# Kernel optimization log

Measured on AMD Instinct MI355X. Metric: run time of the kernel, lower is better.

## Reference

```python
import jax, jax.numpy as jnp
import numpy as np

D_MODEL = 1024
N_HEADS = 16
D_K = D_MODEL // N_HEADS
B, S = 2, 2048


def setup_inputs() -> dict:
    key = jax.random.key(0)
    ks = jax.random.split(key, 9)
    scale = 1.0 / np.sqrt(D_MODEL)
    x = jax.random.normal(ks[0], (B, S, D_MODEL), dtype=jnp.float32)
    # causal mask, broadcastable to [B, H, S, S]; mask==0 -> masked
    mask = jnp.tril(jnp.ones((S, S), dtype=bool))[None, None]
    wq = jax.random.normal(ks[1], (D_MODEL, D_MODEL), dtype=jnp.float32) * scale
    bq = jnp.zeros((D_MODEL,), dtype=jnp.float32)
    wk = jax.random.normal(ks[2], (D_MODEL, D_K), dtype=jnp.float32) * scale
    bk = jnp.zeros((D_K,), dtype=jnp.float32)
    wv = jax.random.normal(ks[3], (D_MODEL, D_K), dtype=jnp.float32) * scale
    bv = jnp.zeros((D_K,), dtype=jnp.float32)
    wo = jax.random.normal(ks[4], (D_MODEL, D_MODEL), dtype=jnp.float32) * scale
    bo = jnp.zeros((D_MODEL,), dtype=jnp.float32)
    return {"x": x, "mask": mask, "wq": wq, "bq": bq, "wk": wk, "bk": bk,
            "wv": wv, "bv": bv, "wo": wo, "bo": bo}


def reference(x, mask, wq, bq, wk, bk, wv, bv, wo, bo):
    b, s, d = x.shape
    h, dk = N_HEADS, D_K
    q = (x @ wq + bq).reshape(b, s, h, dk)            # [b,s,h,dk]
    k = x @ wk + bk                                    # [b,s,dk] shared across heads (MQA)
    v = x @ wv + bv                                    # [b,s,dk]
    scores = jnp.einsum('bshd,btd->bhst', q, k) / jnp.sqrt(jnp.float32(dk))
    scores = jnp.where(mask, scores, jnp.float32(-1e9))
    attn = jax.nn.softmax(scores, axis=-1)             # [b,h,s,t]
    out = jnp.einsum('bhst,btd->bshd', attn, v).reshape(b, s, d)
    return out @ wo + bo
```

## Files before the change

kernel.cpp:

```cpp
#include <hip/hip_runtime.h>
#include <hip/hip_bf16.h>
#include <stdint.h>


typedef __attribute__((ext_vector_type(8))) short short8;
typedef __attribute__((ext_vector_type(4))) short short4_t;
typedef __attribute__((ext_vector_type(4))) float f32x4;

#define MFMA16(a, b, c) __builtin_amdgcn_mfma_f32_16x16x32_bf16((a), (b), (c), 0, 0, 0)

#define SCALE_Q 0.1803368801111244f

__device__ inline void gload_lds16(const void* g, void* l) {
  __builtin_amdgcn_global_load_lds(
      (const __attribute__((address_space(1))) void*)g,
      (__attribute__((address_space(3))) void*)l, 16, 0, 0);
}

__device__ inline float fast_exp2(float x) {
  float r;
  asm("v_exp_f32 %0, %1" : "=v"(r) : "v"(x));
  return r;
}

__device__ inline short f2bf(float f) {
  union { float f; uint32_t u; } v;
  v.f = f;
  uint32_t u = v.u;
  return (short)((u + 0x7fffu + ((u >> 16) & 1u)) >> 16);
}

__device__ inline uint32_t pk_bf16(float lo, float hi) {
  uint32_t r;
  asm("v_cvt_pk_bf16_f32 %0, %1, %2" : "=v"(r) : "v"(lo), "v"(hi));
  return r;
}

__device__ inline int imin(int a, int b) { return a < b ? a : b; }

__global__ __launch_bounds__(256) void k_prep(
    const float* __restrict__ x, const float* __restrict__ wq,
    const float* __restrict__ wk, const float* __restrict__ wv,
    const float* __restrict__ bq, const float* __restrict__ bk,
    const float* __restrict__ bv, const float* __restrict__ wo,
    short* __restrict__ xb, short* __restrict__ wqkvt,
    float* __restrict__ biasq, short* __restrict__ wot) {
  const int blk = blockIdx.x;
  const int t = threadIdx.x;
  if (blk >= 545) {
    const int base = (blk - 545) * 8192;
#pragma unroll
    for (int it = 0; it < 4; ++it) {
      const int i = base + it * 2048 + t * 8;
      const float* xp = x + i;
      short8 o;
#pragma unroll
      for (int j = 0; j < 8; ++j) o[j] = f2bf(xp[j]);
      *(short8*)(xb + i) = o;
    }
    return;
  }
  if (blk == 544) {
    for (int idx = t; idx < 1152; idx += 256)
      biasq[idx] = idx < 1024 ? bq[idx] * SCALE_Q
                              : (idx < 1088 ? bk[idx - 1024] : bv[idx - 1088]);
    return;
  }
  __shared__ float lds[64][65];
  const int j = blk;
  const float* src;
  short* dst;
  int ncol, k0, n0, row0;
  float sc = 1.f;
  if (j < 256)      { src = wq; dst = wqkvt; ncol = 1024; k0 = (j >> 4) * 64;
                      n0 = (j & 15) * 64; row0 = n0; sc = SCALE_Q; }
  else if (j < 272) { src = wk; dst = wqkvt; ncol = 64; k0 = (j - 256) * 64;
                      n0 = 0; row0 = 1024; }
  else if (j < 288) { src = wv; dst = wqkvt; ncol = 64; k0 = (j - 272) * 64;
                      n0 = 0; row0 = 1088; }
  else              { int jj = j - 288; src = wo; dst = wot; ncol = 1024;
                      k0 = (jj >> 4) * 64; n0 = (jj & 15) * 64; row0 = n0; }
#pragma unroll
  for (int i = 0; i < 4; ++i) {
    int f = i * 256 + t;
    int k = f >> 4, c = f & 15;
    const float* sp = src + (size_t)(k0 + k) * ncol + n0 + c * 4;
#pragma unroll
    for (int q = 0; q < 4; ++q) lds[k][c * 4 + q] = sp[q];
  }
  __syncthreads();
#pragma unroll
  for (int i = 0; i < 2; ++i) {
    int f = i * 256 + t;
    int n = f >> 3, kc = f & 7;
    short8 o;
#pragma unroll
    for (int q = 0; q < 8; ++q) o[q] = f2bf(lds[kc * 8 + q][n] * sc);
    *(short8*)(dst + (size_t)(row0 + n) * 1024 + k0 + kc * 8) = o;
  }
}

__global__ __launch_bounds__(256) void k_vt(const short* __restrict__ qkv,
                                            short* __restrict__ vt) {
  __shared__ short lds[64][72];
  const int blk = blockIdx.x;
  const int b = blk >> 5, T = blk & 31;
  const int t = threadIdx.x;
#pragma unroll
  for (int i = 0; i < 2; ++i) {
    int f = i * 256 + t;
    int row = f >> 3, c = f & 7;
    short8 v = *(const short8*)(qkv +
        (size_t)(b * 2048 + T * 64 + row) * 1152 + 1088 + c * 8);
    *(short8*)(&lds[row][c * 8]) = v;
  }
  __syncthreads();
#pragma unroll
  for (int i = 0; i < 2; ++i) {
    int f = i * 256 + t;
    int d = f & 63, g = f >> 6;
    short8 o;
#pragma unroll
    for (int j = 0; j < 8; ++j) {
      int c = g * 8 + j;
      int pi = 16 * ((c >> 1) & 3) + 4 * ((c >> 3) & 3) + 2 * (c >> 5) + (c & 1);
      o[j] = lds[pi][d];
    }
    *(short8*)(vt + (size_t)(b * 64 + d) * 2048 + T * 64 + g * 8) = o;
  }
}

__global__ __launch_bounds__(256, 3) void k_gemm(const short* __restrict__ A,
                                                 const short* __restrict__ Bt,
                                                 const float* __restrict__ bias,
                                                 void* __restrict__ C, int ldc,
                                                 int out_bf16) {
  __shared__ short As[2][4096];
  __shared__ short Bs[2][8192];
  const int t = threadIdx.x;
  const int w = t >> 6, l = t & 63;
  const int l15 = l & 15, lhi = l >> 4;
  const int m0 = blockIdx.x * 64, n0 = blockIdx.y * 128;

  f32x4 acc[4][2];
#pragma unroll
  for (int i = 0; i < 4; ++i)
#pragma unroll
    for (int j = 0; j < 2; ++j)
#pragma unroll
      for (int r = 0; r < 4; ++r) acc[i][j][r] = 0.f;

  const int fA0 = w * 64 + l;
  const int rA0 = fA0 >> 3, gA0 = (fA0 & 7) ^ (rA0 & 7);
  const int fA1 = fA0 + 256;
  const int rA1 = fA1 >> 3, gA1 = (fA1 & 7) ^ (rA1 & 7);

  const int aoff = l15 * 128 + ((lhi ^ (l15 & 7)) << 4);
  const int coff = l15 * 128 + (((4 + lhi) ^ (l15 & 7)) << 4);

#define GEMM_STAGE(buf, k0)                                                    \
  {                                                                            \
    gload_lds16(A + (size_t)(m0 + rA0) * 1024 + (k0) + gA0 * 8,               \
                &As[buf][w * 512]);                                            \
    gload_lds16(A + (size_t)(m0 + rA1) * 1024 + (k0) + gA1 * 8,               \
                &As[buf][2048 + w * 512]);                                     \
    _Pragma("unroll")                                                          \
    for (int q = 0; q < 4; ++q) {                                              \
      int f = q * 256 + fA0;                                                   \
      int r = f >> 3, gc = (f & 7) ^ (r & 7);                                  \
      gload_lds16(Bt + (size_t)(n0 + r) * 1024 + (k0) + gc * 8,               \
                  &Bs[buf][q * 2048 + w * 512]);                               \
    }                                                                          \
  }

  GEMM_STAGE(0, 0);

  for (int ks = 0; ks < 16; ++ks) {
    const int nb = (ks + 1) & 1;
    GEMM_STAGE(nb, imin(ks + 1, 15) * 64);
    asm volatile("s_waitcnt vmcnt(6)" ::: "memory");

    const char* as = (const char*)&As[ks & 1][0];
    const char* bs = (const char*)&Bs[ks & 1][0];
    short8 afA[4], afB[4], bfA[2], bfB[2];
#pragma unroll
    for (int i = 0; i < 4; ++i) {
      afA[i] = *(const short8*)(as + i * 2048 + aoff);
      afB[i] = *(const short8*)(as + i * 2048 + coff);
    }
#pragma unroll
    for (int j = 0; j < 2; ++j) {
      bfA[j] = *(const short8*)(bs + (w * 32 + j * 16) * 128 + aoff);
      bfB[j] = *(const short8*)(bs + (w * 32 + j * 16) * 128 + coff);
    }
#pragma unroll
    for (int i = 0; i < 4; ++i)
#pragma unroll
      for (int j = 0; j < 2; ++j) {
        acc[i][j] = MFMA16(afA[i], bfA[j], acc[i][j]);
        acc[i][j] = MFMA16(afB[i], bfB[j], acc[i][j]);
      }
    __builtin_amdgcn_s_barrier();
  }
  asm volatile("s_waitcnt vmcnt(0)" ::: "memory");

#pragma unroll
  for (int j = 0; j < 2; ++j) {
    int col = n0 + w * 32 + j * 16 + l15;
    float bia = bias[col];
#pragma unroll
    for (int i = 0; i < 4; ++i) {
      int row0 = m0 + i * 16 + lhi * 4;
      if (out_bf16) {
#pragma unroll
        for (int r = 0; r < 4; ++r)
          ((short*)C)[(size_t)(row0 + r) * ldc + col] =
              (short)(pk_bf16(acc[i][j][r] + bia, 0.f) & 0xffff);
      } else {
#pragma unroll
        for (int r = 0; r < 4; ++r)
          ((float*)C)[(size_t)(row0 + r) * ldc + col] = acc[i][j][r] + bia;
      }
    }
  }
#undef GEMM_STAGE
}

__global__ __launch_bounds__(512, 4) void k_attn(const short* __restrict__ qkv,
                                                 const short* __restrict__ vt,
                                                 short* __restrict__ attnb) {
  __shared__ char smem[65536];
  const int t = threadIdx.x;
  const int w = t >> 6, l = t & 63;
  const int l15 = l & 15, lhi = l >> 4;
  const int qw = w & 3, g2 = w >> 2;
  const int bx = blockIdx.x;
  const int o = bx >> 5, gg = o & 7;
  const int p = (o < 8) ? gg : 15 - gg;
  const int bh = bx & 31, b = bh >> 4, h = bh & 15;
  const int ntiles = 2 * p + 2, nph = p + 1;
  const short* kb = qkv + (size_t)(b * 2048) * 1152 + 1024;
  const short* vb = vt + (size_t)b * 64 * 2048;

  const int srow = w * 8 + (l >> 3);
  const int gcol = (l & 7) ^ (l >> 3);
  const short* kS = kb + (size_t)srow * 1152 + gcol * 8;
  const short* vS = vb + (size_t)srow * 2048 + gcol * 8;

  const int aoff = l15 * 128 + ((lhi ^ (l15 & 7)) << 4);
  const int coff = l15 * 128 + (((4 + lhi) ^ (l15 & 7)) << 4);

  short8 ones;
#pragma unroll
  for (int j = 0; j < 8; ++j) ones[j] = (short)0x3F80;

  const int qbase = p * 128 + qw * 32;
  const int myq0 = qbase + l15;
  const int myq1 = qbase + 16 + l15;
  const int ttdiag = qbase >> 6;

  const short* qp0 = qkv + (size_t)(b * 2048 + myq0) * 1152 + h * 64 + 8 * lhi;
  const short* qp1 = qkv + (size_t)(b * 2048 + myq1) * 1152 + h * 64 + 8 * lhi;
  short8 qa0 = *(const short8*)(qp0);
  short8 qc0 = *(const short8*)(qp0 + 32);
  short8 qa1 = *(const short8*)(qp1);
  short8 qc1 = *(const short8*)(qp1 + 32);

  f32x4 oo[2][4], o5a, o5b;
#pragma unroll
  for (int qg = 0; qg < 2; ++qg)
#pragma unroll
    for (int fd = 0; fd < 4; ++fd)
#pragma unroll
      for (int r = 0; r < 4; ++r) oo[qg][fd][r] = 0.f;
#pragma unroll
  for (int r = 0; r < 4; ++r) { o5a[r] = 0.f; o5b[r] = 0.f; }

  gload_lds16(kS, smem + w * 1024);
  gload_lds16(kS + 73728, smem + 16384 + w * 1024);
  gload_lds16(vS, smem + 32768 + w * 1024);
  gload_lds16(vS + 64, smem + 32768 + 16384 + w * 1024);
  __syncthreads();

#pragma unroll 1
  for (int i = 0; i < nph; ++i) {
    if (i + 1 < nph) {
      const int nb = (i + 1) & 1;
      const size_t ko2 = (size_t)(2 * i + 2) * 73728;
      const int vo2 = (2 * i + 2) * 64;
      gload_lds16(kS + ko2, smem + nb * 8192 + w * 1024);
      gload_lds16(kS + ko2 + 73728, smem + 16384 + nb * 8192 + w * 1024);
      gload_lds16(vS + vo2, smem + 32768 + nb * 8192 + w * 1024);
      gload_lds16(vS + vo2 + 64, smem + 32768 + 16384 + nb * 8192 + w * 1024);
      __builtin_amdgcn_sched_barrier(0);
    }

    const int tt = 2 * i + g2;
    const int cb = i & 1;

    const char* kr = smem + g2 * 16384 + cb * 8192;
    f32x4 s0[4], s1[4];
    __builtin_amdgcn_s_setprio(1);
#pragma unroll
    for (int f = 0; f < 4; ++f) {
      short8 ka = *(const short8*)(kr + f * 2048 + aoff);
      short8 kc = *(const short8*)(kr + f * 2048 + coff);
      f32x4 z0 = {0.f, 0.f, 0.f, 0.f};
      z0 = MFMA16(ka, qa0, z0);
      z0 = MFMA16(kc, qc0, z0);
      s0[f] = z0;
      f32x4 z1 = {0.f, 0.f, 0.f, 0.f};
      z1 = MFMA16(ka, qa1, z1);
      z1 = MFMA16(kc, qc1, z1);
      s1[f] = z1;
    }
    __builtin_amdgcn_s_setprio(0);

    if (tt >= ttdiag) {
      const int t0 = tt * 64;
#pragma unroll
      for (int f = 0; f < 4; ++f) {
        int kvb = t0 + f * 16 + lhi * 4;
#pragma unroll
        for (int r = 0; r < 4; ++r) {
          s0[f][r] = (kvb + r <= myq0) ? s0[f][r] : -1e30f;
          s1[f][r] = (kvb + r <= myq1) ? s1[f][r] : -1e30f;
        }
      }
    }

#pragma unroll
    for (int f = 0; f < 4; ++f)
#pragma unroll
      for (int r = 0; r < 4; ++r) {
        s0[f][r] = fast_exp2(s0[f][r]);
        s1[f][r] = fast_exp2(s1[f][r]);
      }

    union { short8 v; uint32_t d[4]; } pA0, pB0, pA1, pB1;
#pragma unroll
    for (int f = 0; f < 4; ++f) {
      pA0.d[f] = pk_bf16(s0[f][0], s0[f][1]);
      pB0.d[f] = pk_bf16(s0[f][2], s0[f][3]);
      pA1.d[f] = pk_bf16(s1[f][0], s1[f][1]);
      pB1.d[f] = pk_bf16(s1[f][2], s1[f][3]);
    }

    const char* vr = smem + 32768 + g2 * 16384 + cb * 8192;
    __builtin_amdgcn_s_setprio(1);
#pragma unroll
    for (int fd = 0; fd < 4; ++fd) {
      short8 va = *(const short8*)(vr + fd * 2048 + aoff);
      short8 vc = *(const short8*)(vr + fd * 2048 + coff);
      oo[0][fd] = MFMA16(va, pA0.v, oo[0][fd]);
      oo[0][fd] = MFMA16(vc, pB0.v, oo[0][fd]);
      oo[1][fd] = MFMA16(va, pA1.v, oo[1][fd]);
      oo[1][fd] = MFMA16(vc, pB1.v, oo[1][fd]);
    }
    o5a = MFMA16(ones, pA0.v, o5a);
    o5a = MFMA16(ones, pB0.v, o5a);
    o5b = MFMA16(ones, pA1.v, o5b);
    o5b = MFMA16(ones, pB1.v, o5b);
    __builtin_amdgcn_s_setprio(0);

    __syncthreads();
  }

  float* scr = (float*)smem;
  float* sp = scr + ((qw << 6) + l) * 34;
  if (g2 == 1) {
#pragma unroll
    for (int qg = 0; qg < 2; ++qg)
#pragma unroll
      for (int fd = 0; fd < 4; ++fd)
#pragma unroll
        for (int r = 0; r < 4; ++r) sp[qg * 16 + fd * 4 + r] = oo[qg][fd][r];
    sp[32] = o5a[0];
    sp[33] = o5b[0];
  }
  __syncthreads();
  if (g2 == 0) {
#pragma unroll
    for (int qg = 0; qg < 2; ++qg) {
      float lsum = (qg ? o5b[0] : o5a[0]) + sp[32 + qg];
      float inv = 1.f / lsum;
      int myq = qbase + qg * 16 + l15;
      short* op = attnb + (size_t)(b * 2048 + myq) * 1024 + h * 64;
#pragma unroll
      for (int fd = 0; fd < 4; ++fd) {
        union { short4_t s4; uint32_t d[2]; } ov;
        float v0 = (oo[qg][fd][0] + sp[qg * 16 + fd * 4 + 0]) * inv;
        float v1 = (oo[qg][fd][1] + sp[qg * 16 + fd * 4 + 1]) * inv;
        float v2 = (oo[qg][fd][2] + sp[qg * 16 + fd * 4 + 2]) * inv;
        float v3 = (oo[qg][fd][3] + sp[qg * 16 + fd * 4 + 3]) * inv;
        ov.d[0] = pk_bf16(v0, v1);
        ov.d[1] = pk_bf16(v2, v3);
        *(short4_t*)(op + fd * 16 + lhi * 4) = ov.s4;
      }
    }
  }
}

extern "C" void kernel_launch(void* const* d_in, const int* in_sizes, int n_in,
                              void* d_out, int out_size, void* d_ws, size_t ws_size,
                              hipStream_t stream) {
  const float* x  = (const float*)d_in[0];
  const float* wq = (const float*)d_in[2];
  const float* bq = (const float*)d_in[3];
  const float* wk = (const float*)d_in[4];
  const float* bk = (const float*)d_in[5];
  const float* wv = (const float*)d_in[6];
  const float* bv = (const float*)d_in[7];
  const float* wo = (const float*)d_in[8];
  const float* bo = (const float*)d_in[9];

  char* ws = (char*)d_ws;
  short* xb    = (short*)(ws + 0);
  short* qkv   = (short*)(ws + 8388608);
  short* wqkvt = (short*)(ws + 17825792);
  short* wot   = (short*)(ws + 20185088);
  short* vt    = (short*)(ws + 22282240);
  short* attnb = (short*)(ws + 22806528);
  float* biasq = (float*)(ws + 31195136);

  k_prep<<<1057, 256, 0, stream>>>(x, wq, wk, wv, bq, bk, bv, wo,
                                   xb, wqkvt, biasq, wot);
  k_gemm<<<dim3(64, 9), 256, 0, stream>>>(xb, wqkvt, biasq, qkv, 1152, 1);
  k_vt<<<64, 256, 0, stream>>>(qkv, vt);
  k_attn<<<512, 512, 0, stream>>>(qkv, vt, attnb);
  k_gemm<<<dim3(64, 8), 256, 0, stream>>>(attnb, wot, bo, d_out, 1024, 0);
}
```

Before: 71.74 us.

## Halve attention block to 4 waves, each computing 64 query rows

The attention kernel drops from 8 waves to 4 waves per block, and each wave now handles 64 query rows (four 16-row groups) instead of 32. K/V fragments loaded from LDS are reused across all four groups, which cuts LDS reads per MFMA. Each wave issues twice the global-to-LDS staging loads. The cost is much higher register pressure from 16 output accumulators plus Q fragments, and fewer waves to hide latency, with launch bounds changed to (256,2).

```diff
diff --git a/kernel.cpp b/kernel.cpp
--- a/kernel.cpp
+++ b/kernel.cpp
@@ -226,26 +226,28 @@
 #undef GEMM_STAGE
 }
 
-__global__ __launch_bounds__(512, 4) void k_attn(const short* __restrict__ qkv,
+__global__ __launch_bounds__(256, 2) void k_attn(const short* __restrict__ qkv,
                                                  const short* __restrict__ vt,
                                                  short* __restrict__ attnb) {
   __shared__ char smem[65536];
   const int t = threadIdx.x;
   const int w = t >> 6, l = t & 63;
   const int l15 = l & 15, lhi = l >> 4;
-  const int qw = w & 3, g2 = w >> 2;
+  const int qw = w & 1, g2 = w >> 1;
   const int bx = blockIdx.x;
   const int o = bx >> 5, gg = o & 7;
   const int p = (o < 8) ? gg : 15 - gg;
   const int bh = bx & 31, b = bh >> 4, h = bh & 15;
-  const int ntiles = 2 * p + 2, nph = p + 1;
+  const int nph = p + 1;
   const short* kb = qkv + (size_t)(b * 2048) * 1152 + 1024;
   const short* vb = vt + (size_t)b * 64 * 2048;
 
-  const int srow = w * 8 + (l >> 3);
+  const int srow = w * 16 + (l >> 3);
   const int gcol = (l & 7) ^ (l >> 3);
   const short* kS = kb + (size_t)srow * 1152 + gcol * 8;
   const short* vS = vb + (size_t)srow * 2048 + gcol * 8;
+  const short* kS2 = kS + (size_t)8 * 1152;
+  const short* vS2 = vS + (size_t)8 * 2048;
 
   const int aoff = l15 * 128 + ((lhi ^ (l15 & 7)) << 4);
   const int coff = l15 * 128 + (((4 + lhi) ^ (l15 & 7)) << 4);
@@ -254,44 +256,51 @@
 #pragma unroll
   for (int j = 0; j < 8; ++j) ones[j] = (short)0x3F80;
 
-  const int qbase = p * 128 + qw * 32;
-  const int myq0 = qbase + l15;
-  const int myq1 = qbase + 16 + l15;
+  const int qbase = p * 128 + qw * 64;
   const int ttdiag = qbase >> 6;
 
-  const short* qp0 = qkv + (size_t)(b * 2048 + myq0) * 1152 + h * 64 + 8 * lhi;
-  const short* qp1 = qkv + (size_t)(b * 2048 + myq1) * 1152 + h * 64 + 8 * lhi;
-  short8 qa0 = *(const short8*)(qp0);
-  short8 qc0 = *(const short8*)(qp0 + 32);
-  short8 qa1 = *(const short8*)(qp1);
-  short8 qc1 = *(const short8*)(qp1 + 32);
-
-  f32x4 oo[2][4], o5a, o5b;
-#pragma unroll
-  for (int qg = 0; qg < 2; ++qg)
+  short8 qa[4], qc[4];
+#pragma unroll
+  for (int g = 0; g < 4; ++g) {
+    const short* qp = qkv +
+        (size_t)(b * 2048 + qbase + g * 16 + l15) * 1152 + h * 64 + 8 * lhi;
+    qa[g] = *(const short8*)(qp);
+    qc[g] = *(const short8*)(qp + 32);
+  }
+
+  f32x4 oo[4][4], o5[4];
+#pragma unroll
+  for (int g = 0; g < 4; ++g) {
 #pragma unroll
     for (int fd = 0; fd < 4; ++fd)
 #pragma unroll
-      for (int r = 0; r < 4; ++r) oo[qg][fd][r] = 0.f;
-#pragma unroll
-  for (int r = 0; r < 4; ++r) { o5a[r] = 0.f; o5b[r] = 0.f; }
-
-  gload_lds16(kS, smem + w * 1024);
-  gload_lds16(kS + 73728, smem + 16384 + w * 1024);
-  gload_lds16(vS, smem + 32768 + w * 1024);
-  gload_lds16(vS + 64, smem + 32768 + 16384 + w * 1024);
+      for (int r = 0; r < 4; ++r) oo[g][fd][r] = 0.f;
+#pragma unroll
+    for (int r = 0; r < 4; ++r) o5[g][r] = 0.f;
+  }
+
+#define ASTAGE(db, tl)                                                         \
+  {                                                                            \
+    const size_t ko = (size_t)(tl) * 73728;                                    \
+    const int vo = (tl) * 64;                                                  \
+    gload_lds16(kS + ko, smem + (db) * 8192 + w * 2048);                       \
+    gload_lds16(kS2 + ko, smem + (db) * 8192 + w * 2048 + 1024);               \
+    gload_lds16(kS + ko + 73728, smem + 16384 + (db) * 8192 + w * 2048);       \
+    gload_lds16(kS2 + ko + 73728,                                              \
+                smem + 16384 + (db) * 8192 + w * 2048 + 1024);                 \
+    gload_lds16(vS + vo, smem + 32768 + (db) * 8192 + w * 2048);               \
+    gload_lds16(vS2 + vo, smem + 32768 + (db) * 8192 + w * 2048 + 1024);       \
+    gload_lds16(vS + vo + 64, smem + 49152 + (db) * 8192 + w * 2048);          \
+    gload_lds16(vS2 + vo + 64, smem + 49152 + (db) * 8192 + w * 2048 + 1024);  \
+  }
+
+  ASTAGE(0, 0);
   __syncthreads();
 
 #pragma unroll 1
   for (int i = 0; i < nph; ++i) {
     if (i + 1 < nph) {
-      const int nb = (i + 1) & 1;
-      const size_t ko2 = (size_t)(2 * i + 2) * 73728;
-      const int vo2 = (2 * i + 2) * 64;
-      gload_lds16(kS + ko2, smem + nb * 8192 + w * 1024);
-      gload_lds16(kS + ko2 + 73728, smem + 16384 + nb * 8192 + w * 1024);
-      gload_lds16(vS + vo2, smem + 32768 + nb * 8192 + w * 1024);
-      gload_lds16(vS + vo2 + 64, smem + 32768 + 16384 + nb * 8192 + w * 1024);
+      ASTAGE((i + 1) & 1, 2 * i + 2);
       __builtin_amdgcn_sched_barrier(0);
     }
 
@@ -299,51 +308,52 @@
     const int cb = i & 1;
 
     const char* kr = smem + g2 * 16384 + cb * 8192;
-    f32x4 s0[4], s1[4];
-    __builtin_amdgcn_s_setprio(1);
+    short8 ka[4], kc[4];
 #pragma unroll
     for (int f = 0; f < 4; ++f) {
-      short8 ka = *(const short8*)(kr + f * 2048 + aoff);
-      short8 kc = *(const short8*)(kr + f * 2048 + coff);
-      f32x4 z0 = {0.f, 0.f, 0.f, 0.f};
-      z0 = MFMA16(ka, qa0, z0);
-      z0 = MFMA16(kc, qc0, z0);
-      s0[f] = z0;
-      f32x4 z1 = {0.f, 0.f, 0.f, 0.f};
-      z1 = MFMA16(ka, qa1, z1);
-      z1 = MFMA16(kc, qc1, z1);
-      s1[f] = z1;
-    }
-    __builtin_amdgcn_s_setprio(0);
-
-    if (tt >= ttdiag) {
-      const int t0 = tt * 64;
+      ka[f] = *(const short8*)(kr + f * 2048 + aoff);
+      kc[f] = *(const short8*)(kr + f * 2048 + coff);
+    }
+
+    union { short8 v; uint32_t d[4]; } pA[4], pB[4];
+    const int t0 = tt * 64;
+
+#pragma unroll
+    for (int g = 0; g < 4; ++g) {
+      f32x4 s[4];
+      __builtin_amdgcn_s_setprio(1);
 #pragma unroll
       for (int f = 0; f < 4; ++f) {
-        int kvb = t0 + f * 16 + lhi * 4;
-#pragma unroll
-        for (int r = 0; r < 4; ++r) {
-          s0[f][r] = (kvb + r <= myq0) ? s0[f][r] : -1e30f;
-          s1[f][r] = (kvb + r <= myq1) ? s1[f][r] : -1e30f;
+        f32x4 z = {0.f, 0.f, 0.f, 0.f};
+        z = MFMA16(ka[f], qa[g], z);
+        z = MFMA16(kc[f], qc[g], z);
+        s[f] = z;
+      }
+      __builtin_amdgcn_s_setprio(0);
+
+      if (tt >= ttdiag) {
+        const int myq = qbase + g * 16 + l15;
+#pragma unroll
+        for (int f = 0; f < 4; ++f) {
+          int kvb = t0 + f * 16 + lhi * 4;
+#pragma unroll
+          for (int r = 0; r < 4; ++r)
+            s[f][r] = (kvb + r <= myq) ? s[f][r] : -1e30f;
         }
       }
-    }
-
-#pragma unroll
-    for (int f = 0; f < 4; ++f)
-#pragma unroll
-      for (int r = 0; r < 4; ++r) {
-        s0[f][r] = fast_exp2(s0[f][r]);
-        s1[f][r] = fast_exp2(s1[f][r]);
-      }
-
-    union { short8 v; uint32_t d[4]; } pA0, pB0, pA1, pB1;
-#pragma unroll
-    for (int f = 0; f < 4; ++f) {
-      pA0.d[f] = pk_bf16(s0[f][0], s0[f][1]);
-      pB0.d[f] = pk_bf16(s0[f][2], s0[f][3]);
-      pA1.d[f] = pk_bf16(s1[f][0], s1[f][1]);
-      pB1.d[f] = pk_bf16(s1[f][2], s1[f][3]);
+
+#pragma unroll
+      for (int f = 0; f < 4; ++f) {
+        s[f][0] = fast_exp2(s[f][0]);
+        s[f][1] = fast_exp2(s[f][1]);
+        s[f][2] = fast_exp2(s[f][2]);
+        s[f][3] = fast_exp2(s[f][3]);
+      }
+#pragma unroll
+      for (int f = 0; f < 4; ++f) {
+        pA[g].d[f] = pk_bf16(s[f][0], s[f][1]);
+        pB[g].d[f] = pk_bf16(s[f][2], s[f][3]);
+      }
     }
 
     const char* vr = smem + 32768 + g2 * 16384 + cb * 8192;
@@ -352,47 +362,50 @@
     for (int fd = 0; fd < 4; ++fd) {
       short8 va = *(const short8*)(vr + fd * 2048 + aoff);
       short8 vc = *(const short8*)(vr + fd * 2048 + coff);
-      oo[0][fd] = MFMA16(va, pA0.v, oo[0][fd]);
-      oo[0][fd] = MFMA16(vc, pB0.v, oo[0][fd]);
-      oo[1][fd] = MFMA16(va, pA1.v, oo[1][fd]);
-      oo[1][fd] = MFMA16(vc, pB1.v, oo[1][fd]);
-    }
-    o5a = MFMA16(ones, pA0.v, o5a);
-    o5a = MFMA16(ones, pB0.v, o5a);
-    o5b = MFMA16(ones, pA1.v, o5b);
-    o5b = MFMA16(ones, pB1.v, o5b);
+#pragma unroll
+      for (int g = 0; g < 4; ++g) {
+        oo[g][fd] = MFMA16(va, pA[g].v, oo[g][fd]);
+        oo[g][fd] = MFMA16(vc, pB[g].v, oo[g][fd]);
+      }
+    }
+#pragma unroll
+    for (int g = 0; g < 4; ++g) {
+      o5[g] = MFMA16(ones, pA[g].v, o5[g]);
+      o5[g] = MFMA16(ones, pB[g].v, o5[g]);
+    }
     __builtin_amdgcn_s_setprio(0);
 
     __syncthreads();
   }
+#undef ASTAGE
 
   float* scr = (float*)smem;
-  float* sp = scr + ((qw << 6) + l) * 34;
+  float* sp = scr + ((qw << 6) + l) * 68;
   if (g2 == 1) {
 #pragma unroll
-    for (int qg = 0; qg < 2; ++qg)
+    for (int g = 0; g < 4; ++g) {
 #pragma unroll
       for (int fd = 0; fd < 4; ++fd)
 #pragma unroll
-        for (int r = 0; r < 4; ++r) sp[qg * 16 + fd * 4 + r] = oo[qg][fd][r];
-    sp[32] = o5a[0];
-    sp[33] = o5b[0];
+        for (int r = 0; r < 4; ++r) sp[g * 16 + fd * 4 + r] = oo[g][fd][r];
+      sp[64 + g] = o5[g][0];
+    }
   }
   __syncthreads();
   if (g2 == 0) {
 #pragma unroll
-    for (int qg = 0; qg < 2; ++qg) {
-      float lsum = (qg ? o5b[0] : o5a[0]) + sp[32 + qg];
+    for (int g = 0; g < 4; ++g) {
+      float lsum = o5[g][0] + sp[64 + g];
       float inv = 1.f / lsum;
-      int myq = qbase + qg * 16 + l15;
+      int myq = qbase + g * 16 + l15;
       short* op = attnb + (size_t)(b * 2048 + myq) * 1024 + h * 64;
 #pragma unroll
       for (int fd = 0; fd < 4; ++fd) {
         union { short4_t s4; uint32_t d[2]; } ov;
-        float v0 = (oo[qg][fd][0] + sp[qg * 16 + fd * 4 + 0]) * inv;
-        float v1 = (oo[qg][fd][1] + sp[qg * 16 + fd * 4 + 1]) * inv;
-        float v2 = (oo[qg][fd][2] + sp[qg * 16 + fd * 4 + 2]) * inv;
-        float v3 = (oo[qg][fd][3] + sp[qg * 16 + fd * 4 + 3]) * inv;
+        float v0 = (oo[g][fd][0] + sp[g * 16 + fd * 4 + 0]) * inv;
+        float v1 = (oo[g][fd][1] + sp[g * 16 + fd * 4 + 1]) * inv;
+        float v2 = (oo[g][fd][2] + sp[g * 16 + fd * 4 + 2]) * inv;
+        float v3 = (oo[g][fd][3] + sp[g * 16 + fd * 4 + 3]) * inv;
         ov.d[0] = pk_bf16(v0, v1);
         ov.d[1] = pk_bf16(v2, v3);
         *(short4_t*)(op + fd * 16 + lhi * 4) = ov.s4;
@@ -427,6 +440,6 @@
                                    xb, wqkvt, biasq, wot);
   k_gemm<<<dim3(64, 9), 256, 0, stream>>>(xb, wqkvt, biasq, qkv, 1152, 1);
   k_vt<<<64, 256, 0, stream>>>(qkv, vt);
-  k_attn<<<512, 512, 0, stream>>>(qkv, vt, attnb);
+  k_attn<<<512, 256, 0, stream>>>(qkv, vt, attnb);
   k_gemm<<<dim3(64, 8), 256, 0, stream>>>(attnb, wot, bo, d_out, 1024, 0);
 }
```

Measured after the change: 72.79 us. No clear change (+1.5%).

## Split attention into smaller 64-query blocks with 32-key tiles and 4 waves

Applied to the files above, without the earlier changes.

The attention kernel now launches 1024 blocks of 256 threads, each handling 64 queries instead of 128. Each iteration processes two 32-key tiles instead of two 64-key tiles, and the V transpose permutation changes to match the new P fragment layout. The aim is finer-grained parallelism, better causal load balancing and lower per-block LDS so more blocks are resident. The cost is more per-block overhead, more synchronisation relative to MFMA work, and more iterations with half the MFMA work each.

```diff
diff --git a/kernel.cpp b/kernel.cpp
--- a/kernel.cpp
+++ b/kernel.cpp
@@ -123,7 +123,7 @@
 #pragma unroll
     for (int j = 0; j < 8; ++j) {
       int c = g * 8 + j;
-      int pi = 16 * ((c >> 1) & 3) + 4 * ((c >> 3) & 3) + 2 * (c >> 5) + (c & 1);
+      int pi = 32 * (c >> 5) + 16 * ((c >> 2) & 1) + 4 * ((c >> 3) & 3) + (c & 3);
       o[j] = lds[pi][d];
     }
     *(short8*)(vt + (size_t)(b * 64 + d) * 2048 + T * 64 + g * 8) = o;
@@ -226,26 +226,26 @@
 #undef GEMM_STAGE
 }
 
-__global__ __launch_bounds__(512, 4) void k_attn(const short* __restrict__ qkv,
+__global__ __launch_bounds__(256, 4) void k_attn(const short* __restrict__ qkv,
                                                  const short* __restrict__ vt,
                                                  short* __restrict__ attnb) {
-  __shared__ char smem[65536];
+  __shared__ char smem[32768];
   const int t = threadIdx.x;
   const int w = t >> 6, l = t & 63;
   const int l15 = l & 15, lhi = l >> 4;
-  const int qw = w & 3, g2 = w >> 2;
+  const int qw = w & 1, g2 = w >> 1;
   const int bx = blockIdx.x;
-  const int o = bx >> 5, gg = o & 7;
-  const int p = (o < 8) ? gg : 15 - gg;
+  const int o = bx >> 5, g = o & 7;
+  const int cc = (o < 8) ? g : (o < 16) ? 15 - g : (o < 24) ? 16 + g : 31 - g;
   const int bh = bx & 31, b = bh >> 4, h = bh & 15;
-  const int ntiles = 2 * p + 2, nph = p + 1;
+  const int nph = cc + 1;
   const short* kb = qkv + (size_t)(b * 2048) * 1152 + 1024;
   const short* vb = vt + (size_t)b * 64 * 2048;
 
-  const int srow = w * 8 + (l >> 3);
   const int gcol = (l & 7) ^ (l >> 3);
-  const short* kS = kb + (size_t)srow * 1152 + gcol * 8;
-  const short* vS = vb + (size_t)srow * 2048 + gcol * 8;
+  const short* kS = kb + (size_t)(w * 8 + (l >> 3)) * 1152 + gcol * 8;
+  const short* vS1 = vb + (size_t)(w * 16 + (l >> 3)) * 2048 + gcol * 8;
+  const short* vS2 = vS1 + (size_t)8 * 2048;
 
   const int aoff = l15 * 128 + ((lhi ^ (l15 & 7)) << 4);
   const int coff = l15 * 128 + (((4 + lhi) ^ (l15 & 7)) << 4);
@@ -254,10 +254,10 @@
 #pragma unroll
   for (int j = 0; j < 8; ++j) ones[j] = (short)0x3F80;
 
-  const int qbase = p * 128 + qw * 32;
+  const int qbase = cc * 64 + qw * 32;
   const int myq0 = qbase + l15;
   const int myq1 = qbase + 16 + l15;
-  const int ttdiag = qbase >> 6;
+  const int ttdiag = qbase >> 5;
 
   const short* qp0 = qkv + (size_t)(b * 2048 + myq0) * 1152 + h * 64 + 8 * lhi;
   const short* qp1 = qkv + (size_t)(b * 2048 + myq1) * 1152 + h * 64 + 8 * lhi;
@@ -276,33 +276,33 @@
 #pragma unroll
   for (int r = 0; r < 4; ++r) { o5a[r] = 0.f; o5b[r] = 0.f; }
 
-  gload_lds16(kS, smem + w * 1024);
-  gload_lds16(kS + 73728, smem + 16384 + w * 1024);
-  gload_lds16(vS, smem + 32768 + w * 1024);
-  gload_lds16(vS + 64, smem + 32768 + 16384 + w * 1024);
+#define ASTAGE(db, tl, G)                                                      \
+  {                                                                            \
+    gload_lds16(kS + (size_t)(tl) * 36864, smem + (db) * 4096 + w * 1024);     \
+    gload_lds16(kS + (size_t)((tl) + 1) * 36864,                               \
+                smem + 8192 + (db) * 4096 + w * 1024);                         \
+    gload_lds16(vS1 + (G) * 64, smem + 16384 + (db) * 8192 + w * 2048);        \
+    gload_lds16(vS2 + (G) * 64, smem + 16384 + (db) * 8192 + w * 2048 + 1024); \
+  }
+
+  ASTAGE(0, 0, 0);
   __syncthreads();
 
 #pragma unroll 1
   for (int i = 0; i < nph; ++i) {
     if (i + 1 < nph) {
-      const int nb = (i + 1) & 1;
-      const size_t ko2 = (size_t)(2 * i + 2) * 73728;
-      const int vo2 = (2 * i + 2) * 64;
-      gload_lds16(kS + ko2, smem + nb * 8192 + w * 1024);
-      gload_lds16(kS + ko2 + 73728, smem + 16384 + nb * 8192 + w * 1024);
-      gload_lds16(vS + vo2, smem + 32768 + nb * 8192 + w * 1024);
-      gload_lds16(vS + vo2 + 64, smem + 32768 + 16384 + nb * 8192 + w * 1024);
+      ASTAGE((i + 1) & 1, 2 * i + 2, i + 1);
       __builtin_amdgcn_sched_barrier(0);
     }
 
     const int tt = 2 * i + g2;
     const int cb = i & 1;
 
-    const char* kr = smem + g2 * 16384 + cb * 8192;
-    f32x4 s0[4], s1[4];
+    const char* kr = smem + g2 * 8192 + cb * 4096;
+    f32x4 s0[2], s1[2];
     __builtin_amdgcn_s_setprio(1);
 #pragma unroll
-    for (int f = 0; f < 4; ++f) {
+    for (int f = 0; f < 2; ++f) {
       short8 ka = *(const short8*)(kr + f * 2048 + aoff);
       short8 kc = *(const short8*)(kr + f * 2048 + coff);
       f32x4 z0 = {0.f, 0.f, 0.f, 0.f};
@@ -317,9 +317,9 @@
     __builtin_amdgcn_s_setprio(0);
 
     if (tt >= ttdiag) {
-      const int t0 = tt * 64;
-#pragma unroll
-      for (int f = 0; f < 4; ++f) {
+      const int t0 = tt * 32;
+#pragma unroll
+      for (int f = 0; f < 2; ++f) {
         int kvb = t0 + f * 16 + lhi * 4;
 #pragma unroll
         for (int r = 0; r < 4; ++r) {
@@ -330,41 +330,39 @@
     }
 
 #pragma unroll
-    for (int f = 0; f < 4; ++f)
+    for (int f = 0; f < 2; ++f)
 #pragma unroll
       for (int r = 0; r < 4; ++r) {
         s0[f][r] = fast_exp2(s0[f][r]);
         s1[f][r] = fast_exp2(s1[f][r]);
       }
 
-    union { short8 v; uint32_t d[4]; } pA0, pB0, pA1, pB1;
-#pragma unroll
-    for (int f = 0; f < 4; ++f) {
-      pA0.d[f] = pk_bf16(s0[f][0], s0[f][1]);
-      pB0.d[f] = pk_bf16(s0[f][2], s0[f][3]);
-      pA1.d[f] = pk_bf16(s1[f][0], s1[f][1]);
-      pB1.d[f] = pk_bf16(s1[f][2], s1[f][3]);
-    }
-
-    const char* vr = smem + 32768 + g2 * 16384 + cb * 8192;
+    union { short8 v; uint32_t d[4]; } pA0, pA1;
+    pA0.d[0] = pk_bf16(s0[0][0], s0[0][1]);
+    pA0.d[1] = pk_bf16(s0[0][2], s0[0][3]);
+    pA0.d[2] = pk_bf16(s0[1][0], s0[1][1]);
+    pA0.d[3] = pk_bf16(s0[1][2], s0[1][3]);
+    pA1.d[0] = pk_bf16(s1[0][0], s1[0][1]);
+    pA1.d[1] = pk_bf16(s1[0][2], s1[0][3]);
+    pA1.d[2] = pk_bf16(s1[1][0], s1[1][1]);
+    pA1.d[3] = pk_bf16(s1[1][2], s1[1][3]);
+
+    const char* vr = smem + 16384 + cb * 8192;
+    const int voff = g2 ? coff : aoff;
     __builtin_amdgcn_s_setprio(1);
 #pragma unroll
     for (int fd = 0; fd < 4; ++fd) {
-      short8 va = *(const short8*)(vr + fd * 2048 + aoff);
-      short8 vc = *(const short8*)(vr + fd * 2048 + coff);
+      short8 va = *(const short8*)(vr + fd * 2048 + voff);
       oo[0][fd] = MFMA16(va, pA0.v, oo[0][fd]);
-      oo[0][fd] = MFMA16(vc, pB0.v, oo[0][fd]);
       oo[1][fd] = MFMA16(va, pA1.v, oo[1][fd]);
-      oo[1][fd] = MFMA16(vc, pB1.v, oo[1][fd]);
     }
     o5a = MFMA16(ones, pA0.v, o5a);
-    o5a = MFMA16(ones, pB0.v, o5a);
     o5b = MFMA16(ones, pA1.v, o5b);
-    o5b = MFMA16(ones, pB1.v, o5b);
     __builtin_amdgcn_s_setprio(0);
 
     __syncthreads();
   }
+#undef ASTAGE
 
   float* scr = (float*)smem;
   float* sp = scr + ((qw << 6) + l) * 34;
@@ -427,6 +425,6 @@
                                    xb, wqkvt, biasq, wot);
   k_gemm<<<dim3(64, 9), 256, 0, stream>>>(xb, wqkvt, biasq, qkv, 1152, 1);
   k_vt<<<64, 256, 0, stream>>>(qkv, vt);
-  k_attn<<<512, 512, 0, stream>>>(qkv, vt, attnb);
+  k_attn<<<1024, 256, 0, stream>>>(qkv, vt, attnb);
   k_gemm<<<dim3(64, 8), 256, 0, stream>>>(attnb, wot, bo, d_out, 1024, 0);
 }
```

Measured after the change: 75.16 us. +4.8%, slower.
